# Kernel optimization log

Hardware: AMD Instinct MI355X
Metric: run time of the kernel (lower is better)

The kernel has to match this reference:

```python
import jax, jax.numpy as jnp
import numpy as np

N, n, m, k = 100000, 32, 16, 32
MU = 100.0  # bubble kernel scale (init arg mu)


def setup_inputs() -> dict:
    key = jax.random.key(0)
    ks = jax.random.split(key, 7)
    x = jax.random.normal(ks[0], (N,), dtype=jnp.float32)
    # torch.nn.Linear(N, n): weight [n, N], bias [n]
    encoder_w = jax.random.normal(ks[1], (n, N), dtype=jnp.float32) / np.float32(np.sqrt(N))
    encoder_b = jnp.zeros((n,), dtype=jnp.float32)
    # decoder parameter [n, N]
    decoder = jax.random.normal(ks[2], (n, N), dtype=jnp.float32) / np.float32(np.sqrt(n))
    # torch.nn.Linear(n, n*m): weight [n*m, n], bias [n*m]
    bw_w = jax.random.normal(ks[3], (n * m, n), dtype=jnp.float32) / np.float32(np.sqrt(n))
    bw_b = jnp.zeros((n * m,), dtype=jnp.float32)
    neighbour_distance = jax.random.uniform(ks[4], (N, k), dtype=jnp.float32)
    neighbour_id = jax.random.randint(ks[5], (N, k), 0, N)
    clustering_labels = jax.random.randint(ks[6], (N,), 0, m)
    return {
        "x": x,
        "encoder_w": encoder_w,
        "encoder_b": encoder_b,
        "decoder": decoder,
        "bw_w": bw_w,
        "bw_b": bw_b,
        "neighbour_distance": neighbour_distance,
        "neighbour_id": neighbour_id,
        "clustering_labels": clustering_labels,
    }


def reference(x, encoder_w, encoder_b, decoder, bw_w, bw_b,
              neighbour_distance, neighbour_id, clustering_labels):
    # encode: [N] -> [n]
    encoded = x @ encoder_w.T + encoder_b
    # per-basis, per-cluster bandwidths: sigmoid(Linear)/60 -> [n, m] -> expand to [n, N]
    bandwidths = jax.nn.sigmoid(encoded @ bw_w.T + bw_b) / 60.0
    w = bandwidths.reshape(n, m)[:, clustering_labels]  # [n, N]
    # bubble window: relu(1 - d^2 / (w*mu)^2) -> [n, N, k]
    window = jax.nn.relu(1.0 - neighbour_distance[None, :, :] ** 2
                         / (w[:, :, None] * MU) ** 2)
    # normalization over axis 1 (the N axis), faithful to the source's dim=1
    window = window / jnp.sum(window, axis=1, keepdims=True)
    # gather decoder rows at neighbours, weight, reduce over k: [n, N]
    convolved_basis = jnp.sum(decoder[:, neighbour_id] * window, axis=-1)
    # [n] @ [n, N] -> [N]
    return encoded @ convolved_basis
```

## Files before the change

kernel.cpp:

```cpp
#include <hip/hip_runtime.h>
#include <hip/hip_fp16.h>

#define N_PTS 100000
#define MU_F  100.0f

typedef unsigned int uint;
typedef _Float16 h2 __attribute__((ext_vector_type(2)));
typedef float f2 __attribute__((ext_vector_type(2)));

#define E_SCALE 16384.0f
#define E_SCALE_INV (1.0f / 16384.0f)

static __device__ inline h2 h2pack(float a, float b) {
    return __builtin_bit_cast(h2, __builtin_amdgcn_cvt_pkrtz(a, b));
}
static __device__ inline float fdot2f(h2 a, h2 b, float c) {
    return __builtin_amdgcn_fdot2(a, b, c, false);
}
static __device__ inline h2 h2fma(h2 a, h2 b, h2 c) {
#if __has_builtin(__builtin_elementwise_fma)
    return __builtin_elementwise_fma(a, b, c);
#else
    return a * b + c;
#endif
}
static __device__ inline h2 h2max(h2 a, h2 b) {
#if __has_builtin(__builtin_elementwise_max)
    return __builtin_elementwise_max(a, b);
#else
    h2 r;
    r.x = a.x > b.x ? a.x : b.x;
    r.y = a.y > b.y ? a.y : b.y;
    return r;
#endif
}

#define ENC_BLKS 256
#define TR_BLKS  1563
#define S_BLKS   1024
#define S_PCH    98
#define NPAIRS   (N_PTS / 2)
#define M_BLKS   2048
#define M_CH     ((NPAIRS + M_BLKS - 1) / M_BLKS)

__global__ __launch_bounds__(256) void k_prep(const float* __restrict__ x,
                                              const float* __restrict__ encW,
                                              const float* __restrict__ encB,
                                              float* __restrict__ enc) {
    int b = blockIdx.x;
    int row = b & 31;
    int chunk = b >> 5;
    const int CH = N_PTS / 8;
    int base = chunk * CH;
    const float4* W4 = reinterpret_cast<const float4*>(encW + (size_t)row * N_PTS + base);
    const float4* x4 = reinterpret_cast<const float4*>(x + base);
    const int nv = CH / 4;
    float acc = 0.f;
    for (int idx = threadIdx.x; idx < nv; idx += 256) {
        float4 w = W4[idx];
        float4 xv = x4[idx];
        acc += w.x * xv.x + w.y * xv.y + w.z * xv.z + w.w * xv.w;
    }
    #pragma unroll
    for (int off = 32; off > 0; off >>= 1) acc += __shfl_down(acc, off);
    __shared__ float sred[4];
    int wid = threadIdx.x >> 6;
    if ((threadIdx.x & 63) == 0) sred[wid] = acc;
    __syncthreads();
    if (threadIdx.x == 0) {
        float s = sred[0] + sred[1] + sred[2] + sred[3];
        if (chunk == 0) s += encB[row];
        atomicAdd(enc + row, s);
    }
}

__global__ __launch_bounds__(256) void k_tab(const float* __restrict__ enc_g,
                                             const float* __restrict__ bw_w,
                                             const float* __restrict__ bw_b,
                                             float* __restrict__ invFG,
                                             h2* __restrict__ invHLG) {
    __shared__ float encL[32];
    __shared__ float invF[512];
    if (threadIdx.x < 32) encL[threadIdx.x] = enc_g[threadIdx.x];
    __syncthreads();
    for (int r = threadIdx.x; r < 512; r += 256) {
        int i = r >> 4, c = r & 15;
        const float4* wr4 = reinterpret_cast<const float4*>(bw_w + (size_t)r * 32);
        float z = bw_b[r];
        #pragma unroll
        for (int p4 = 0; p4 < 8; ++p4) {
            float4 wv = wr4[p4];
            z = fmaf(encL[4 * p4 + 0], wv.x, z);
            z = fmaf(encL[4 * p4 + 1], wv.y, z);
            z = fmaf(encL[4 * p4 + 2], wv.z, z);
            z = fmaf(encL[4 * p4 + 3], wv.w, z);
        }
        float s = 1.f / (1.f + __expf(-z));
        float wmu = s * (MU_F / 60.0f);
        float iv = 1.f / (wmu * wmu);
        invF[c * 32 + i] = iv;
        invFG[c * 32 + i] = iv;
    }
    __syncthreads();
    {
        int t = threadIdx.x;
        int c = t >> 4, q = (t >> 2) & 3, tt = t & 3;
        int i0 = q * 8 + 2 * tt;
        invHLG[t] = h2pack(fminf(invF[c * 32 + i0], 6.0e4f),
                           fminf(invF[c * 32 + i0 + 1], 6.0e4f));
    }
}

__global__ __launch_bounds__(256, 4) void k_S(const float* __restrict__ invFG,
                                              const float* __restrict__ nd,
                                              const int* __restrict__ labels,
                                              float* __restrict__ S,
                                              float* __restrict__ S_part,
                                              const float* __restrict__ dec,
                                              __half* __restrict__ decT) {
    int b = blockIdx.x;
    if (b >= S_BLKS) {
        __shared__ float tile[32][65];
        int j0 = (b - S_BLKS) * 64;
        int col = threadIdx.x & 63;
        int r0 = threadIdx.x >> 6;
        #pragma unroll
        for (int it = 0; it < 8; ++it) {
            int row = it * 4 + r0;
            int j = j0 + col;
            float v = (j < N_PTS) ? dec[(size_t)row * N_PTS + j] : 0.f;
            tile[row][col] = v;
        }
        __syncthreads();
        #pragma unroll
        for (int it = 0; it < 4; ++it) {
            int idx = it * 256 + threadIdx.x;
            int j = idx >> 4;
            int p = idx & 15;
            int jj = j0 + j;
            if (jj < N_PTS) {
                __half2 h = __halves2half2(__float2half(tile[2 * p][j]),
                                           __float2half(tile[2 * p + 1][j]));
                *reinterpret_cast<__half2*>(decT + (size_t)jj * 32 + 2 * p) = h;
            }
        }
        return;
    }

    __shared__ float invF[512];
    if (threadIdx.x < 128)
        reinterpret_cast<float4*>(invF)[threadIdx.x] =
            reinterpret_cast<const float4*>(invFG)[threadIdx.x];
    __syncthreads();

    int kk = threadIdx.x & 31;
    int ig = threadIdx.x >> 5;
    int start = b * S_PCH;
    int jend = min(start + S_PCH, N_PTS);

    float a0 = 0.f, a1 = 0.f, a2 = 0.f, a3 = 0.f;

    auto ld4 = [&](int jbase, float* d, int* cc) {
        #pragma unroll
        for (int u = 0; u < 4; ++u) {
            int j = jbase + u;
            int jc = min(j, N_PTS - 1);
            float dv = nd[(size_t)jc * 32 + kk];
            cc[u] = labels[jc];
            d[u] = (j < jend) ? dv : 1.0e15f;
        }
    };
    float dA[4], dB[4]; int cA[4], cB[4];
    ld4(start, dA, cA);
    for (int jj = start; jj < jend; jj += 4) {
        ld4(jj + 4, dB, cB);
        #pragma unroll
        for (int u = 0; u < 4; ++u) {
            float4 iv = *reinterpret_cast<const float4*>(&invF[cA[u] * 32 + ig * 4]);
            float d2 = dA[u] * dA[u];
            a0 += fmaxf(fmaf(d2, -iv.x, 1.f), 0.f);
            a1 += fmaxf(fmaf(d2, -iv.y, 1.f), 0.f);
            a2 += fmaxf(fmaf(d2, -iv.z, 1.f), 0.f);
            a3 += fmaxf(fmaf(d2, -iv.w, 1.f), 0.f);
        }
        #pragma unroll
        for (int u = 0; u < 4; ++u) { dA[u] = dB[u]; cA[u] = cB[u]; }
    }

    int cell = (ig * 4) * 32 + kk;
    if (S_part) {
        float* dst = S_part + (size_t)b * 1024 + cell;
        dst[0] = a0; dst[32] = a1; dst[64] = a2; dst[96] = a3;
    } else {
        atomicAdd(&S[cell], a0);
        atomicAdd(&S[cell + 32], a1);
        atomicAdd(&S[cell + 64], a2);
        atomicAdd(&S[cell + 96], a3);
    }
}

__global__ __launch_bounds__(1024) void k_S_reduce(const float* __restrict__ S_part,
                                                   float* __restrict__ S) {
    int g = blockIdx.x;
    int t = threadIdx.x;
    float s = 0.f;
    #pragma unroll
    for (int u = 0; u < 16; ++u)
        s += S_part[(size_t)(g * 16 + u) * 1024 + t];
    atomicAdd(&S[t], s);
}

__global__ __launch_bounds__(256) void k_elf(const float* __restrict__ enc_g,
                                             const float* __restrict__ S_g,
                                             h2* __restrict__ EhG_A,
                                             h2* __restrict__ EhG_B) {
    __shared__ float encL[32];
    __shared__ float ELf[1024];
    if (threadIdx.x < 32) encL[threadIdx.x] = enc_g[threadIdx.x];
    __syncthreads();
    for (int t = threadIdx.x; t < 1024; t += 256)
        ELf[t] = encL[t >> 5] / S_g[t] * E_SCALE;
    __syncthreads();
    {
        int t = threadIdx.x;
        int lane = t >> 2, tt = t & 3;
        int R = lane >> 2, q = lane & 3;
        int i0 = q * 8 + 2 * tt;
        EhG_A[t] = h2pack(ELf[i0 * 32 + R],      ELf[(i0 + 1) * 32 + R]);
        EhG_B[t] = h2pack(ELf[i0 * 32 + R + 16], ELf[(i0 + 1) * 32 + R + 16]);
    }
}

__global__ __launch_bounds__(256, 4) void k_main(const h2* __restrict__ invHLG,
                                                 const h2* __restrict__ EhG_A,
                                                 const h2* __restrict__ EhG_B,
                                                 const float* __restrict__ nd,
                                                 const int* __restrict__ nid,
                                                 const int* __restrict__ labels,
                                                 const __half* __restrict__ decT,
                                                 float* __restrict__ out) {
    __shared__ h2 invHL[256];
    if (threadIdx.x < 64)
        reinterpret_cast<uint4*>(invHL)[threadIdx.x] =
            reinterpret_cast<const uint4*>(invHLG)[threadIdx.x];
    __syncthreads();

    int lane = threadIdx.x & 63;
    int R = lane >> 2;
    int q = lane & 3;

    h2 EhA[4], EhB[4];
    {
        uint4 a = reinterpret_cast<const uint4*>(EhG_A)[lane];
        uint4 bq = reinterpret_cast<const uint4*>(EhG_B)[lane];
        EhA[0] = __builtin_bit_cast(h2, a.x);  EhA[1] = __builtin_bit_cast(h2, a.y);
        EhA[2] = __builtin_bit_cast(h2, a.z);  EhA[3] = __builtin_bit_cast(h2, a.w);
        EhB[0] = __builtin_bit_cast(h2, bq.x); EhB[1] = __builtin_bit_cast(h2, bq.y);
        EhB[2] = __builtin_bit_cast(h2, bq.z); EhB[3] = __builtin_bit_cast(h2, bq.w);
    }
    const h2 zero2 = h2pack(0.f, 0.f);
    const h2 one2 = h2pack(1.f, 1.f);

    int w = threadIdx.x >> 6;
    int start = blockIdx.x * M_CH;
    int pend = min(start + M_CH, NPAIRS);
    int pa = start + w;
    const uint4* decQ = reinterpret_cast<const uint4*>(decT);
    if (pa >= pend) return;

    auto load_ldd = [&](int pc, int* id, float* dd, int& c0, int& c1) {
        pc = min(pc, NPAIRS - 1);
        int j0 = 2 * pc, j1 = j0 + 1;
        #pragma unroll
        for (int s = 0; s < 4; ++s) {
            size_t idx = (size_t)((s >> 1) ? j1 : j0) * 32 + (s & 1) * 16 + R;
            id[s] = __builtin_nontemporal_load(&nid[idx]);
            dd[s] = __builtin_nontemporal_load(&nd[idx]);
        }
        c0 = labels[j0];
        c1 = labels[j1];
    };
    auto load_rows = [&](const int* id, uint4* r) {
        #pragma unroll
        for (int s = 0; s < 4; ++s)
            r[s] = decQ[(size_t)id[s] * 4 + q];
    };
    auto load_ih = [&](int c0, int c1, h2* ih0, h2* ih1) {
        uint4 a = *reinterpret_cast<const uint4*>(&invHL[c0 * 16 + q * 4]);
        uint4 bq = *reinterpret_cast<const uint4*>(&invHL[c1 * 16 + q * 4]);
        ih0[0] = __builtin_bit_cast(h2, a.x);  ih0[1] = __builtin_bit_cast(h2, a.y);
        ih0[2] = __builtin_bit_cast(h2, a.z);  ih0[3] = __builtin_bit_cast(h2, a.w);
        ih1[0] = __builtin_bit_cast(h2, bq.x); ih1[1] = __builtin_bit_cast(h2, bq.y);
        ih1[2] = __builtin_bit_cast(h2, bq.z); ih1[3] = __builtin_bit_cast(h2, bq.w);
    };

    int ida[4], idb[4]; float dda[4], ddb[4];
    int ca0, ca1, cb0, cb1;
    uint4 ra[4], rb[4];
    h2 ihA0[4], ihA1[4];

    load_ldd(pa, ida, dda, ca0, ca1);
    load_ldd(pa + 4, idb, ddb, cb0, cb1);
    load_rows(ida, ra);
    load_ih(ca0, ca1, ihA0, ihA1);

    while (pa < pend) {
        load_rows(idb, rb);
        h2 ihB0[4], ihB1[4];
        load_ih(cb0, cb1, ihB0, ihB1);
        int idc[4]; float ddc[4]; int cc0, cc1;
        load_ldd(pa + 8, idc, ddc, cc0, cc1);
        __builtin_amdgcn_sched_barrier(0);

        float d20 = dda[0] * dda[0];
        float d21 = dda[1] * dda[1];
        float d22 = dda[2] * dda[2];
        float d23 = dda[3] * dda[3];
        h2 md0 = h2pack(-d20, -d20);
        h2 md1 = h2pack(-d21, -d21);
        h2 md2 = h2pack(-d22, -d22);
        h2 md3 = h2pack(-d23, -d23);

        float a0 = 0.f, a1 = 0.f, a2 = 0.f, a3 = 0.f;
        #pragma unroll
        for (int t = 0; t < 4; ++t) {
            uint dw0 = (t == 0) ? ra[0].x : (t == 1) ? ra[0].y : (t == 2) ? ra[0].z : ra[0].w;
            uint dw1 = (t == 0) ? ra[1].x : (t == 1) ? ra[1].y : (t == 2) ? ra[1].z : ra[1].w;
            uint dw2 = (t == 0) ? ra[2].x : (t == 1) ? ra[2].y : (t == 2) ? ra[2].z : ra[2].w;
            uint dw3 = (t == 0) ? ra[3].x : (t == 1) ? ra[3].y : (t == 2) ? ra[3].z : ra[3].w;
            {
                h2 wv = h2max(h2fma(md0, ihA0[t], one2), zero2);
                a0 = fdot2f(wv * EhA[t], __builtin_bit_cast(h2, dw0), a0);
            }
            {
                h2 wv = h2max(h2fma(md1, ihA0[t], one2), zero2);
                a1 = fdot2f(wv * EhB[t], __builtin_bit_cast(h2, dw1), a1);
            }
            {
                h2 wv = h2max(h2fma(md2, ihA1[t], one2), zero2);
                a2 = fdot2f(wv * EhA[t], __builtin_bit_cast(h2, dw2), a2);
            }
            {
                h2 wv = h2max(h2fma(md3, ihA1[t], one2), zero2);
                a3 = fdot2f(wv * EhB[t], __builtin_bit_cast(h2, dw3), a3);
            }
        }
        float u = a0 + a1;
        float v = a2 + a3;
        #pragma unroll
        for (int off = 32; off > 0; off >>= 1) {
            u += __shfl_xor(u, off);
            v += __shfl_xor(v, off);
        }
        if (lane == 0)  out[2 * pa]     = u * E_SCALE_INV;
        if (lane == 32) out[2 * pa + 1] = v * E_SCALE_INV;

        ca0 = cb0; ca1 = cb1; cb0 = cc0; cb1 = cc1;
        #pragma unroll
        for (int s = 0; s < 4; ++s) {
            dda[s] = ddb[s]; ddb[s] = ddc[s];
            ida[s] = idb[s]; idb[s] = idc[s];
            ra[s] = rb[s];
            ihA0[s] = ihB0[s]; ihA1[s] = ihB1[s];
        }
        pa += 4;
    }
}

extern "C" void kernel_launch(void* const* d_in, const int* in_sizes, int n_in,
                              void* d_out, int out_size, void* d_ws, size_t ws_size,
                              hipStream_t stream) {
    const float* x     = (const float*)d_in[0];
    const float* enc_w = (const float*)d_in[1];
    const float* enc_b = (const float*)d_in[2];
    const float* dec   = (const float*)d_in[3];
    const float* bw_w  = (const float*)d_in[4];
    const float* bw_b  = (const float*)d_in[5];
    const float* nd    = (const float*)d_in[6];
    const int*   nid   = (const int*)d_in[7];
    const int*   labels= (const int*)d_in[8];
    float* out = (float*)d_out;

    char* ws = (char*)d_ws;
    float* enc    = (float*)(ws + 0);
    float* S      = (float*)(ws + 128);
    float* invFG  = (float*)(ws + 4224);
    h2*    invHLG = (h2*)(ws + 6272);
    h2*    EhG_A  = (h2*)(ws + 7296);
    h2*    EhG_B  = (h2*)(ws + 8320);
    __half* decT  = (__half*)(ws + 532480);
    bool use_part = ws_size >= 11126784ull;
    float* S_part = use_part ? (float*)(ws + 6932480) : nullptr;

    (void)hipMemsetAsync(d_ws, 0, 4224, stream);
    k_prep<<<dim3(ENC_BLKS), dim3(256), 0, stream>>>(x, enc_w, enc_b, enc);
    k_tab<<<dim3(1), dim3(256), 0, stream>>>(enc, bw_w, bw_b, invFG, invHLG);
    k_S<<<dim3(S_BLKS + TR_BLKS), dim3(256), 0, stream>>>(
        invFG, nd, labels, S, S_part, dec, decT);
    if (use_part)
        k_S_reduce<<<dim3(64), dim3(1024), 0, stream>>>(S_part, S);
    k_elf<<<dim3(1), dim3(256), 0, stream>>>(enc, S, EhG_A, EhG_B);
    k_main<<<dim3(M_BLKS), dim3(256), 0, stream>>>(invHLG, EhG_A, EhG_B,
                                                   nd, nid, labels, decT, out);
}
```

Measured before the change: 174.7 us.

## Drop S partial-reduce and elf kernels, fold scaling into main, deepen prefetch

Removes the k_S_reduce and k_elf launches. k_S now always adds its partial sums into S with atomics, and k_main computes its scaled encoder/S half-precision coefficients itself at block start. k_S adds a third prefetch stage and nontemporal loads of the distances, occupancy hints change (k_S to 8, k_main to 6 blocks per CU), and the scheduling barrier in k_main is removed. This cuts two launches and their serialization, at the cost of atomic contention on 1024 cells from 1024 blocks, redundant per-thread divisions in k_main, and possible register pressure from the higher occupancy targets.

```diff
diff --git a/kernel.cpp b/kernel.cpp
--- a/kernel.cpp
+++ b/kernel.cpp
@@ -42,6 +42,7 @@
 #define NPAIRS   (N_PTS / 2)
 #define M_BLKS   2048
 #define M_CH     ((NPAIRS + M_BLKS - 1) / M_BLKS)
+
 
 __global__ __launch_bounds__(256) void k_prep(const float* __restrict__ x,
                                               const float* __restrict__ encW,
@@ -111,11 +112,10 @@
     }
 }
 
-__global__ __launch_bounds__(256, 4) void k_S(const float* __restrict__ invFG,
+__global__ __launch_bounds__(256, 8) void k_S(const float* __restrict__ invFG,
                                               const float* __restrict__ nd,
                                               const int* __restrict__ labels,
                                               float* __restrict__ S,
-                                              float* __restrict__ S_part,
                                               const float* __restrict__ dec,
                                               __half* __restrict__ decT) {
     int b = blockIdx.x;
@@ -165,15 +165,16 @@
         for (int u = 0; u < 4; ++u) {
             int j = jbase + u;
             int jc = min(j, N_PTS - 1);
-            float dv = nd[(size_t)jc * 32 + kk];
+            float dv = __builtin_nontemporal_load(&nd[(size_t)jc * 32 + kk]);
             cc[u] = labels[jc];
             d[u] = (j < jend) ? dv : 1.0e15f;
         }
     };
-    float dA[4], dB[4]; int cA[4], cB[4];
+    float dA[4], dB[4], dC[4]; int cA[4], cB[4], cC[4];
     ld4(start, dA, cA);
+    ld4(start + 4, dB, cB);
     for (int jj = start; jj < jend; jj += 4) {
-        ld4(jj + 4, dB, cB);
+        ld4(jj + 8, dC, cC);
         #pragma unroll
         for (int u = 0; u < 4; ++u) {
             float4 iv = *reinterpret_cast<const float4*>(&invF[cA[u] * 32 + ig * 4]);
@@ -184,56 +185,22 @@
             a3 += fmaxf(fmaf(d2, -iv.w, 1.f), 0.f);
         }
         #pragma unroll
-        for (int u = 0; u < 4; ++u) { dA[u] = dB[u]; cA[u] = cB[u]; }
+        for (int u = 0; u < 4; ++u) {
+            dA[u] = dB[u]; cA[u] = cB[u];
+            dB[u] = dC[u]; cB[u] = cC[u];
+        }
     }
 
     int cell = (ig * 4) * 32 + kk;
-    if (S_part) {
-        float* dst = S_part + (size_t)b * 1024 + cell;
-        dst[0] = a0; dst[32] = a1; dst[64] = a2; dst[96] = a3;
-    } else {
-        atomicAdd(&S[cell], a0);
-        atomicAdd(&S[cell + 32], a1);
-        atomicAdd(&S[cell + 64], a2);
-        atomicAdd(&S[cell + 96], a3);
-    }
-}
-
-__global__ __launch_bounds__(1024) void k_S_reduce(const float* __restrict__ S_part,
-                                                   float* __restrict__ S) {
-    int g = blockIdx.x;
-    int t = threadIdx.x;
-    float s = 0.f;
-    #pragma unroll
-    for (int u = 0; u < 16; ++u)
-        s += S_part[(size_t)(g * 16 + u) * 1024 + t];
-    atomicAdd(&S[t], s);
-}
-
-__global__ __launch_bounds__(256) void k_elf(const float* __restrict__ enc_g,
-                                             const float* __restrict__ S_g,
-                                             h2* __restrict__ EhG_A,
-                                             h2* __restrict__ EhG_B) {
-    __shared__ float encL[32];
-    __shared__ float ELf[1024];
-    if (threadIdx.x < 32) encL[threadIdx.x] = enc_g[threadIdx.x];
-    __syncthreads();
-    for (int t = threadIdx.x; t < 1024; t += 256)
-        ELf[t] = encL[t >> 5] / S_g[t] * E_SCALE;
-    __syncthreads();
-    {
-        int t = threadIdx.x;
-        int lane = t >> 2, tt = t & 3;
-        int R = lane >> 2, q = lane & 3;
-        int i0 = q * 8 + 2 * tt;
-        EhG_A[t] = h2pack(ELf[i0 * 32 + R],      ELf[(i0 + 1) * 32 + R]);
-        EhG_B[t] = h2pack(ELf[i0 * 32 + R + 16], ELf[(i0 + 1) * 32 + R + 16]);
-    }
-}
-
-__global__ __launch_bounds__(256, 4) void k_main(const h2* __restrict__ invHLG,
-                                                 const h2* __restrict__ EhG_A,
-                                                 const h2* __restrict__ EhG_B,
+    atomicAdd(&S[cell], a0);
+    atomicAdd(&S[cell + 32], a1);
+    atomicAdd(&S[cell + 64], a2);
+    atomicAdd(&S[cell + 96], a3);
+}
+
+__global__ __launch_bounds__(256, 6) void k_main(const h2* __restrict__ invHLG,
+                                                 const float* __restrict__ enc_g,
+                                                 const float* __restrict__ S_g,
                                                  const float* __restrict__ nd,
                                                  const int* __restrict__ nid,
                                                  const int* __restrict__ labels,
@@ -250,13 +217,14 @@
     int q = lane & 3;
 
     h2 EhA[4], EhB[4];
-    {
-        uint4 a = reinterpret_cast<const uint4*>(EhG_A)[lane];
-        uint4 bq = reinterpret_cast<const uint4*>(EhG_B)[lane];
-        EhA[0] = __builtin_bit_cast(h2, a.x);  EhA[1] = __builtin_bit_cast(h2, a.y);
-        EhA[2] = __builtin_bit_cast(h2, a.z);  EhA[3] = __builtin_bit_cast(h2, a.w);
-        EhB[0] = __builtin_bit_cast(h2, bq.x); EhB[1] = __builtin_bit_cast(h2, bq.y);
-        EhB[2] = __builtin_bit_cast(h2, bq.z); EhB[3] = __builtin_bit_cast(h2, bq.w);
+    #pragma unroll
+    for (int t = 0; t < 4; ++t) {
+        int i0 = q * 8 + 2 * t;
+        float e0 = enc_g[i0], e1 = enc_g[i0 + 1];
+        float sA0 = S_g[i0 * 32 + R],      sA1 = S_g[(i0 + 1) * 32 + R];
+        float sB0 = S_g[i0 * 32 + R + 16], sB1 = S_g[(i0 + 1) * 32 + R + 16];
+        EhA[t] = h2pack(e0 / sA0 * E_SCALE, e1 / sA1 * E_SCALE);
+        EhB[t] = h2pack(e0 / sB0 * E_SCALE, e1 / sB1 * E_SCALE);
     }
     const h2 zero2 = h2pack(0.f, 0.f);
     const h2 one2 = h2pack(1.f, 1.f);
@@ -310,7 +278,6 @@
         load_ih(cb0, cb1, ihB0, ihB1);
         int idc[4]; float ddc[4]; int cc0, cc1;
         load_ldd(pa + 8, idc, ddc, cc0, cc1);
-        __builtin_amdgcn_sched_barrier(0);
 
         float d20 = dda[0] * dda[0];
         float d21 = dda[1] * dda[1];
@@ -386,20 +353,13 @@
     float* S      = (float*)(ws + 128);
     float* invFG  = (float*)(ws + 4224);
     h2*    invHLG = (h2*)(ws + 6272);
-    h2*    EhG_A  = (h2*)(ws + 7296);
-    h2*    EhG_B  = (h2*)(ws + 8320);
     __half* decT  = (__half*)(ws + 532480);
-    bool use_part = ws_size >= 11126784ull;
-    float* S_part = use_part ? (float*)(ws + 6932480) : nullptr;
 
     (void)hipMemsetAsync(d_ws, 0, 4224, stream);
     k_prep<<<dim3(ENC_BLKS), dim3(256), 0, stream>>>(x, enc_w, enc_b, enc);
     k_tab<<<dim3(1), dim3(256), 0, stream>>>(enc, bw_w, bw_b, invFG, invHLG);
     k_S<<<dim3(S_BLKS + TR_BLKS), dim3(256), 0, stream>>>(
-        invFG, nd, labels, S, S_part, dec, decT);
-    if (use_part)
-        k_S_reduce<<<dim3(64), dim3(1024), 0, stream>>>(S_part, S);
-    k_elf<<<dim3(1), dim3(256), 0, stream>>>(enc, S, EhG_A, EhG_B);
-    k_main<<<dim3(M_BLKS), dim3(256), 0, stream>>>(invHLG, EhG_A, EhG_B,
-                                                   nd, nid, labels, decT, out);
-}
+        invFG, nd, labels, S, dec, decT);
+    k_main<<<dim3(M_BLKS), dim3(256), 0, stream>>>(invHLG, enc, S, nd, nid,
+                                                   labels, decT, out);
+}
```

Result: slower. 189.3 us (+8.3%).
